# Kernel optimization log

Hardware: AMD Instinct MI355X
Metric: run time of the kernel (lower is better)

Reference implementation:

```python
import jax, jax.numpy as jnp
import numpy as np

C = 256
CK = C // 8  # query/key projection dim

def conv1x1(x, w, b):
    # x: (B,C,H,W), w: (O,C), b: (O,)
    return jnp.einsum('bchw,oc->bohw', x, w) + b[None, :, None, None]

def conv3x3(x, w, b):
    # w: (O,C,3,3)
    y = jax.lax.conv_general_dilated(x, w, window_strides=(1, 1), padding='SAME',
                                     dimension_numbers=('NCHW', 'OIHW', 'NCHW'))
    return y + b[None, :, None, None]

def setup_inputs() -> dict:
    key = jax.random.key(0)
    ks = jax.random.split(key, 24)
    s = 0.05
    d = {
        'x1': jax.random.normal(ks[0], (4, C, 64, 64), jnp.float32),
        'x2': jax.random.normal(ks[1], (4, C, 64, 64), jnp.float32),
        'wq1': jax.random.normal(ks[2], (CK, C), jnp.float32) * s,
        'bq1': jax.random.normal(ks[3], (CK,), jnp.float32) * s,
        'wk1': jax.random.normal(ks[4], (CK, C), jnp.float32) * s,
        'bk1': jax.random.normal(ks[5], (CK,), jnp.float32) * s,
        'wv1': jax.random.normal(ks[6], (C, C), jnp.float32) * s,
        'bv1': jax.random.normal(ks[7], (C,), jnp.float32) * s,
        'wq2': jax.random.normal(ks[8], (CK, C), jnp.float32) * s,
        'bq2': jax.random.normal(ks[9], (CK,), jnp.float32) * s,
        'wk2': jax.random.normal(ks[10], (CK, C), jnp.float32) * s,
        'bk2': jax.random.normal(ks[11], (CK,), jnp.float32) * s,
        'wv2': jax.random.normal(ks[12], (C, C), jnp.float32) * s,
        'bv2': jax.random.normal(ks[13], (C,), jnp.float32) * s,
        'wd1': jax.random.normal(ks[14], (C, C), jnp.float32) * s,
        'bd1': jax.random.normal(ks[15], (C,), jnp.float32) * s,
        'wd3': jax.random.normal(ks[16], (C, C, 3, 3), jnp.float32) * s,
        'bd3': jax.random.normal(ks[17], (C,), jnp.float32) * s,
        'gamma1': jax.random.normal(ks[18], (1,), jnp.float32) * 0.5,
        'gamma2': jax.random.normal(ks[19], (1,), jnp.float32) * 0.5,
    }
    return d

def reference(x1, x2, wq1, bq1, wk1, bk1, wv1, bv1, wq2, bq2, wk2, bk2, wv2, bv2,
              wd1, bd1, wd3, bd3, gamma1, gamma2):
    B, Cc, H, W = x1.shape
    N = H * W
    # projections (1x1 convs), flattened to (B, d, N)
    q1 = conv1x1(x1, wq1, bq1).reshape(B, CK, N)
    k1 = conv1x1(x1, wk1, bk1).reshape(B, CK, N)
    v1 = conv1x1(x1, wv1, bv1).reshape(B, Cc, N)
    q2 = conv1x1(x2, wq2, bq2).reshape(B, CK, N)
    k2 = conv1x1(x2, wk2, bk2).reshape(B, CK, N)
    v2 = conv1x1(x2, wv2, bv2).reshape(B, Cc, N)
    # cross attention 1: queries from x1, keys/values from x2
    energy1 = jnp.einsum('bdi,bdj->bij', q1, k2)          # (B,N,N)
    attn1 = jax.nn.softmax(energy1, axis=-1)
    out1 = jnp.einsum('bcj,bij->bci', v2, attn1).reshape(B, Cc, H, W)
    # cross attention 2: queries from x2, keys/values from x1
    energy2 = jnp.einsum('bdi,bdj->bij', q2, k1)
    attn2 = jax.nn.softmax(energy2, axis=-1)
    out2 = jnp.einsum('bcj,bij->bci', v1, attn2).reshape(B, Cc, H, W)
    # residual conv branches + gamma-scaled skip (norm1/norm2 in source are dead code)
    out1 = out1 + conv1x1(x1, wd1, bd1) + conv3x3(x1, wd3, bd3)
    out2 = out2 + conv1x1(x2, wd1, bd1) + conv3x3(x2, wd3, bd3)
    out1 = x1 + gamma1[0] * out1
    out2 = x2 + gamma2[0] * out2
    return (out1, out2)
```

## Files before the change

### kernel.cpp

```cpp
#include <hip/hip_runtime.h>
#include <hip/hip_bf16.h>

#define CC 256
#define CKD 32
#define NN 4096
#define HH 64
#define WW 64
#define BB 4

#define LOG2E 1.44269504088896f
#define EXPSHIFT 23.0831203874f

typedef __attribute__((ext_vector_type(8))) short short8;
typedef __attribute__((ext_vector_type(4))) float floatx4;

__device__ __forceinline__ unsigned f2bf(float f) {
  union { float f; unsigned u; } v; v.f = f;
  unsigned r = v.u + 0x7fffu + ((v.u >> 16) & 1u);
  return r >> 16;
}
__device__ __forceinline__ unsigned short f2bf_fast(float f) {
  return (unsigned short)((__float_as_uint(f) + 0x8000u) >> 16);
}
__device__ __forceinline__ float fast_exp2(float x) {
#if __has_builtin(__builtin_amdgcn_exp2f)
  return __builtin_amdgcn_exp2f(x);
#else
  return __expf(x * 0.693147181f);
#endif
}

__global__ __launch_bounds__(256) void xpack_kernel(
    const float* __restrict__ x1, const float* __restrict__ x2,
    unsigned short* __restrict__ Xp) {
  const int t = threadIdx.x;
  const int nb = blockIdx.x, cbk = blockIdx.y, img = blockIdx.z;
  const float* X = ((img >> 2) ? x2 : x1) + (size_t)(img & 3) * CC * NN;
  const int n0 = nb * 64, c0 = cbk * 64;
  __shared__ float tile[64][65];
  const int nl = t & 63, cl0 = t >> 6;
#pragma unroll
  for (int i = 0; i < 16; ++i)
    tile[cl0 + i * 4][nl] = X[(size_t)(c0 + cl0 + i * 4) * NN + n0 + nl];
  __syncthreads();
#pragma unroll
  for (int it = 0; it < 2; ++it) {
    int id = it * 256 + t;
    int nl2 = id >> 3, cc = id & 7;
    short8 v;
#pragma unroll
    for (int j = 0; j < 8; ++j) v[j] = (short)f2bf(tile[cc * 8 + j][nl2]);
    *(short8*)(Xp + (size_t)img * NN * CC + (size_t)(n0 + nl2) * CC + c0 + cc * 8) = v;
  }
}

__global__ __launch_bounds__(256) void wpack_kernel(
    const float* __restrict__ wd1, const float* __restrict__ wd3,
    const float* __restrict__ wq1, const float* __restrict__ wk1,
    const float* __restrict__ wv1,
    const float* __restrict__ wq2, const float* __restrict__ wk2,
    const float* __restrict__ wv2,
    const float* __restrict__ bq1, const float* __restrict__ bk1,
    const float* __restrict__ bv1,
    const float* __restrict__ bq2, const float* __restrict__ bk2,
    const float* __restrict__ bv2,
    unsigned short* __restrict__ Wp, unsigned short* __restrict__ Wqkv,
    float* __restrict__ Bias) {
  const int id = blockIdx.x * 256 + threadIdx.x;
#pragma unroll
  for (int tap = 0; tap < 10; ++tap) {
    float v = (tap < 9) ? wd3[(size_t)id * 9 + tap] : wd1[id];
    Wp[(size_t)tap * (CC * CC) + id] = (unsigned short)f2bf(v);
  }
#pragma unroll
  for (int j = 0; j < 3; ++j) {
    int e = id + j * 65536;
    if (e < 2 * 320 * 256) {
      int inp = e / (320 * 256), rem = e % (320 * 256);
      int o = rem >> 8, c = rem & 255;
      float v;
      if (inp == 0)
        v = (o < 32) ? wq1[o * 256 + c] * LOG2E
            : (o < 64) ? wk1[(o - 32) * 256 + c] : wv1[(o - 64) * 256 + c];
      else
        v = (o < 32) ? wq2[o * 256 + c] * LOG2E
            : (o < 64) ? wk2[(o - 32) * 256 + c] : wv2[(o - 64) * 256 + c];
      Wqkv[e] = (unsigned short)f2bf(v);
    }
  }
  if (id < 640) {
    int inp = id / 320, o = id % 320;
    float v;
    if (inp == 0) v = (o < 32) ? bq1[o] * LOG2E
                      : (o < 64) ? bk1[o - 32] : bv1[o - 64];
    else          v = (o < 32) ? bq2[o] * LOG2E
                      : (o < 64) ? bk2[o - 32] : bv2[o - 64];
    Bias[id] = v;
  }
}

__global__ __launch_bounds__(256) void proj_mfma_kernel(
    const unsigned short* __restrict__ Xp, const unsigned short* __restrict__ Wqkv,
    const float* __restrict__ Bias,
    unsigned short* __restrict__ Qp1, unsigned short* __restrict__ Kp1,
    unsigned short* __restrict__ Vp1,
    unsigned short* __restrict__ Qp2, unsigned short* __restrict__ Kp2,
    unsigned short* __restrict__ Vp2) {
  const int t = threadIdx.x;
  const int w = t >> 6, lane = t & 63;
  const int l15 = lane & 15, g = lane >> 4;
  const int img = blockIdx.x, pb = blockIdx.y;
  const int pix0 = pb * 64;
  const int inp = img >> 2, b = img & 3;
  const unsigned short* Xi = Xp + (size_t)img * NN * CC;
  const unsigned short* Wb = Wqkv + (size_t)inp * 320 * CC;
  const float* Bi = Bias + inp * 320;
  unsigned short* Qp = (inp ? Qp2 : Qp1) + (size_t)b * NN * CKD;
  unsigned short* Kp = (inp ? Kp2 : Kp1) + (size_t)b * NN * CKD;
  unsigned short* Vp = (inp ? Vp2 : Vp1) + (size_t)b * NN * CC;

  __shared__ unsigned short tile[320][72];

  floatx4 acc[4][5];
#pragma unroll
  for (int mf = 0; mf < 4; ++mf)
#pragma unroll
    for (int nf = 0; nf < 5; ++nf) acc[mf][nf] = (floatx4){0.f, 0.f, 0.f, 0.f};
  const int o0w = w * 80;

#pragma unroll
  for (int cb = 0; cb < 8; ++cb) {
    short8 a[4], bfr[5];
#pragma unroll
    for (int mf = 0; mf < 4; ++mf)
      a[mf] = *(const short8*)(Xi + (size_t)(pix0 + mf * 16 + l15) * CC + cb * 32 + g * 8);
#pragma unroll
    for (int nf = 0; nf < 5; ++nf)
      bfr[nf] = *(const short8*)(Wb + (size_t)(o0w + nf * 16 + l15) * CC + cb * 32 + g * 8);
#pragma unroll
    for (int nf = 0; nf < 5; ++nf)
#pragma unroll
      for (int mf = 0; mf < 4; ++mf)
        acc[mf][nf] = __builtin_amdgcn_mfma_f32_16x16x32_bf16(
            a[mf], bfr[nf], acc[mf][nf], 0, 0, 0);
  }

#pragma unroll
  for (int nf = 0; nf < 5; ++nf) {
    float bs = Bi[o0w + nf * 16 + l15];
#pragma unroll
    for (int mf = 0; mf < 4; ++mf) {
      uint2 pk;
      pk.x = f2bf(acc[mf][nf][0] + bs) | (f2bf(acc[mf][nf][1] + bs) << 16);
      pk.y = f2bf(acc[mf][nf][2] + bs) | (f2bf(acc[mf][nf][3] + bs) << 16);
      *(uint2*)&tile[o0w + nf * 16 + l15][mf * 16 + g * 4] = pk;
    }
  }
  __syncthreads();

  {
    const int pix = t >> 2, ch = t & 3;
    short8 vq, vk;
#pragma unroll
    for (int e = 0; e < 8; ++e) {
      vq[e] = (short)tile[ch * 8 + e][pix];
      vk[e] = (short)tile[32 + ch * 8 + e][pix];
    }
    *(short8*)(Qp + (size_t)(pix0 + pix) * CKD + ch * 8) = vq;
    *(short8*)(Kp + (size_t)(pix0 + pix) * CKD + ch * 8) = vk;
  }
#pragma unroll
  for (int it = 0; it < 8; ++it) {
    short8 vv = *(const short8*)&tile[64 + t][it * 8];
    *(short8*)(Vp + ((size_t)((pix0 >> 3) + it) * CC + t) * 8) = vv;
  }
}

__global__ __launch_bounds__(256, 2) void conv_mfma_kernel(
    const unsigned short* __restrict__ Xp, const unsigned short* __restrict__ Wp,
    const float* __restrict__ bd1, const float* __restrict__ bd3,
    unsigned short* __restrict__ R1, unsigned short* __restrict__ R2) {
  const int t = threadIdx.x;
  const int w = t >> 6, lane = t & 63;
  const int l15 = lane & 15, g = lane >> 4;
  const int ob = blockIdx.x, img = blockIdx.y, pb = blockIdx.z;
  const int o0 = ob * 128, n0 = pb * 128, y0 = pb * 2;
  const int wm = w >> 1, wn = w & 1;

  const unsigned short* Xi = Xp + (size_t)img * NN * CC;
  unsigned short* R = ((img >> 2) ? R2 : R1) + (size_t)(img & 3) * CC * NN;

  __shared__ unsigned short xs[4][66][72];

  floatx4 acc[4][4];
#pragma unroll
  for (int m = 0; m < 4; ++m)
#pragma unroll
    for (int n = 0; n < 4; ++n) acc[m][n] = (floatx4){0.f, 0.f, 0.f, 0.f};

  for (int cb = 0; cb < 4; ++cb) {
    const int c0 = cb * 64;
    __syncthreads();
#pragma unroll
    for (int it = 0; it < 9; ++it) {
      int id = it * 256 + t;
      if (id < 2112) {
        int r = id / 528, rem = id % 528;
        int col = rem >> 3, cc = rem & 7;
        int y = y0 - 1 + r, x = col - 1;
        short8 v = {0, 0, 0, 0, 0, 0, 0, 0};
        if (y >= 0 && y < HH && x >= 0 && x < WW)
          v = *(const short8*)(Xi + (size_t)(y * WW + x) * CC + c0 + cc * 8);
        *(short8*)&xs[r][col][cc * 8] = v;
      }
    }
    __syncthreads();
#pragma unroll
    for (int tap = 0; tap < 10; ++tap) {
      const int dy = (tap < 9) ? tap / 3 - 1 : 0;
      const int dx = (tap < 9) ? tap % 3 - 1 : 0;
      const int rrow = 1 + wn + dy;
      const unsigned short* wrow =
          Wp + (size_t)(tap * CC + o0 + wm * 64 + l15) * CC + c0 + g * 8;
#pragma unroll
      for (int ks = 0; ks < 2; ++ks) {
        short8 af[4], bf[4];
#pragma unroll
        for (int m = 0; m < 4; ++m)
          af[m] = *(const short8*)(wrow + (size_t)(m * 16) * CC + ks * 32);
#pragma unroll
        for (int n = 0; n < 4; ++n)
          bf[n] = *(const short8*)&xs[rrow][1 + n * 16 + l15 + dx][ks * 32 + g * 8];
#pragma unroll
        for (int m = 0; m < 4; ++m)
#pragma unroll
          for (int n = 0; n < 4; ++n)
            acc[m][n] = __builtin_amdgcn_mfma_f32_16x16x32_bf16(
                af[m], bf[n], acc[m][n], 0, 0, 0);
      }
    }
  }

#pragma unroll
  for (int m = 0; m < 4; ++m) {
    int ob2 = o0 + wm * 64 + m * 16 + g * 4;
    float bs[4];
#pragma unroll
    for (int r = 0; r < 4; ++r) bs[r] = bd1[ob2 + r] + bd3[ob2 + r];
#pragma unroll
    for (int n = 0; n < 4; ++n) {
      int pix = n0 + wn * 64 + n * 16 + l15;
#pragma unroll
      for (int r = 0; r < 4; ++r)
        R[(size_t)(ob2 + r) * NN + pix] = f2bf_fast(acc[m][n][r] + bs[r]);
    }
  }
}

__global__ __launch_bounds__(256, 2) void attn_kernel(
    const unsigned short* __restrict__ Qp1, const unsigned short* __restrict__ Kp1,
    const unsigned short* __restrict__ Qp2, const unsigned short* __restrict__ Kp2,
    const unsigned short* __restrict__ Vp1, const unsigned short* __restrict__ Vp2,
    const unsigned short* __restrict__ R1, const unsigned short* __restrict__ R2,
    const float* __restrict__ x1, const float* __restrict__ x2,
    const float* __restrict__ g1, const float* __restrict__ g2,
    float* __restrict__ out) {
  const int t = threadIdx.x;
  const int w = t >> 6, lane = t & 63;
  const int l15 = lane & 15, g = lane >> 4;
  const int att = blockIdx.x, b = blockIdx.y;
  const int i0 = blockIdx.z * 64;

  const unsigned short *Qp, *Kp, *Vp, *Rb; const float *x; float gamma; float* o;
  if (att == 0) { Qp = Qp1; Kp = Kp2; Vp = Vp2; Rb = R1; x = x1; gamma = g1[0]; o = out; }
  else          { Qp = Qp2; Kp = Kp1; Vp = Vp1; Rb = R2; x = x2; gamma = g2[0];
                  o = out + (size_t)BB * CC * NN; }
  Qp += (size_t)b * NN * CKD; Kp += (size_t)b * NN * CKD; Vp += (size_t)b * NN * CC;
  Rb += (size_t)b * CC * NN; x += (size_t)b * CC * NN; o += (size_t)b * CC * NN;

  __shared__ unsigned short p_s[2][64][72];
  __shared__ float l_s[64];

  short8 bq = *(const short8*)(Qp + (size_t)(i0 + w * 16 + l15) * CKD + g * 8);

  floatx4 acc[4][4];
#pragma unroll
  for (int a = 0; a < 4; ++a)
#pragma unroll
    for (int c = 0; c < 4; ++c) acc[a][c] = (floatx4){0.f, 0.f, 0.f, 0.f};
  float l_acc = 0.f;
  const floatx4 zinit = {-EXPSHIFT, -EXPSHIFT, -EXPSHIFT, -EXPSHIFT};

  short8 kr[2][4], vr[2][8];
#pragma unroll
  for (int js = 0; js < 4; ++js)
    kr[0][js] = *(const short8*)(Kp + (size_t)(js * 16 + l15) * CKD + g * 8);
#pragma unroll
  for (int ks = 0; ks < 2; ++ks)
#pragma unroll
    for (int cs = 0; cs < 4; ++cs)
      vr[0][ks * 4 + cs] = *(const short8*)(Vp +
          ((size_t)(ks * 4 + g) * CC + (w * 64 + cs * 16 + l15)) * 8);

#pragma unroll 2
  for (int jt = 0; jt < NN / 64; ++jt) {
    const int cur = jt & 1, nxt = cur ^ 1;
    if (jt + 1 < NN / 64) {
      const size_t j0n = (size_t)(jt + 1) * 64;
#pragma unroll
      for (int js = 0; js < 4; ++js)
        kr[nxt][js] = *(const short8*)(Kp + (j0n + js * 16 + l15) * CKD + g * 8);
#pragma unroll
      for (int ks = 0; ks < 2; ++ks)
#pragma unroll
        for (int cs = 0; cs < 4; ++cs)
          vr[nxt][ks * 4 + cs] = *(const short8*)(Vp +
              (((j0n >> 3) + ks * 4 + g) * CC + (w * 64 + cs * 16 + l15)) * 8);
    }
#pragma unroll
    for (int js = 0; js < 4; ++js) {
      floatx4 s = __builtin_amdgcn_mfma_f32_16x16x32_bf16(kr[cur][js], bq, zinit, 0, 0, 0);
      float p0 = fast_exp2(s[0]);
      float p1 = fast_exp2(s[1]);
      float p2 = fast_exp2(s[2]);
      float p3 = fast_exp2(s[3]);
      l_acc += (p0 + p1) + (p2 + p3);
      unsigned u0 = __float_as_uint(p0) + 0x8000u;
      unsigned u1 = __float_as_uint(p1) + 0x8000u;
      unsigned u2 = __float_as_uint(p2) + 0x8000u;
      unsigned u3 = __float_as_uint(p3) + 0x8000u;
      uint2 pk;
      pk.x = __builtin_amdgcn_perm(u1, u0, 0x07060302u);
      pk.y = __builtin_amdgcn_perm(u3, u2, 0x07060302u);
      *(uint2*)&p_s[cur][w * 16 + l15][js * 16 + g * 4] = pk;
    }
    __syncthreads();
#pragma unroll
    for (int ks = 0; ks < 2; ++ks) {
      short8 ap[4];
#pragma unroll
      for (int isub = 0; isub < 4; ++isub)
        ap[isub] = *(const short8*)&p_s[cur][isub * 16 + l15][ks * 32 + g * 8];
#pragma unroll
      for (int cs = 0; cs < 4; ++cs)
#pragma unroll
        for (int isub = 0; isub < 4; ++isub)
          acc[isub][cs] = __builtin_amdgcn_mfma_f32_16x16x32_bf16(
              ap[isub], vr[cur][ks * 4 + cs], acc[isub][cs], 0, 0, 0);
    }
  }

  l_acc += __shfl_xor(l_acc, 16);
  l_acc += __shfl_xor(l_acc, 32);
  if (g == 0) l_s[w * 16 + l15] = l_acc;
  __syncthreads();

#pragma unroll
  for (int isub = 0; isub < 4; ++isub) {
    float linv[4];
#pragma unroll
    for (int r = 0; r < 4; ++r) linv[r] = 1.f / l_s[isub * 16 + g * 4 + r];
#pragma unroll
    for (int cs = 0; cs < 4; ++cs) {
      int c = w * 64 + cs * 16 + l15;
      size_t base = (size_t)c * NN + i0 + isub * 16 + g * 4;
      float4 xr = *(const float4*)(x + base);
      uint2 rr = *(const uint2*)(Rb + base);
      float r0 = __uint_as_float(rr.x << 16);
      float r1 = __uint_as_float(rr.x & 0xffff0000u);
      float r2 = __uint_as_float(rr.y << 16);
      float r3 = __uint_as_float(rr.y & 0xffff0000u);
      float4 ov;
      ov.x = xr.x + gamma * (acc[isub][cs][0] * linv[0] + r0);
      ov.y = xr.y + gamma * (acc[isub][cs][1] * linv[1] + r1);
      ov.z = xr.z + gamma * (acc[isub][cs][2] * linv[2] + r2);
      ov.w = xr.w + gamma * (acc[isub][cs][3] * linv[3] + r3);
      *(float4*)(o + base) = ov;
    }
  }
}

extern "C" void kernel_launch(void* const* d_in, const int* in_sizes, int n_in,
                              void* d_out, int out_size, void* d_ws, size_t ws_size,
                              hipStream_t stream) {
  const float* x1  = (const float*)d_in[0];
  const float* x2  = (const float*)d_in[1];
  const float* wq1 = (const float*)d_in[2];
  const float* bq1 = (const float*)d_in[3];
  const float* wk1 = (const float*)d_in[4];
  const float* bk1 = (const float*)d_in[5];
  const float* wv1 = (const float*)d_in[6];
  const float* bv1 = (const float*)d_in[7];
  const float* wq2 = (const float*)d_in[8];
  const float* bq2 = (const float*)d_in[9];
  const float* wk2 = (const float*)d_in[10];
  const float* bk2 = (const float*)d_in[11];
  const float* wv2 = (const float*)d_in[12];
  const float* bv2 = (const float*)d_in[13];
  const float* wd1 = (const float*)d_in[14];
  const float* bd1 = (const float*)d_in[15];
  const float* wd3 = (const float*)d_in[16];
  const float* bd3 = (const float*)d_in[17];
  const float* g1  = (const float*)d_in[18];
  const float* g2  = (const float*)d_in[19];
  float* out = (float*)d_out;

  const size_t QB = (size_t)BB * NN * CKD * 2;
  const size_t VB = (size_t)BB * NN * CC * 2;
  const size_t RB = (size_t)BB * NN * CC * 2;
  const size_t XB = (size_t)2 * BB * NN * CC * 2;
  const size_t WPB = (size_t)10 * CC * CC * 2;
  const size_t WQB = (size_t)2 * 320 * CC * 2;
  char* base = (char*)d_ws;
  unsigned short* R1 = (unsigned short*)(base);
  unsigned short* R2 = (unsigned short*)(base + RB);
  unsigned short* Qp1 = (unsigned short*)(base + 2 * RB);
  unsigned short* Kp1 = (unsigned short*)(base + 2 * RB + QB);
  unsigned short* Qp2 = (unsigned short*)(base + 2 * RB + 2 * QB);
  unsigned short* Kp2 = (unsigned short*)(base + 2 * RB + 3 * QB);
  unsigned short* Vp1 = (unsigned short*)(base + 2 * RB + 4 * QB);
  unsigned short* Vp2 = (unsigned short*)(base + 2 * RB + 4 * QB + VB);
  unsigned short* Xp  = (unsigned short*)(base + 2 * RB + 4 * QB + 2 * VB);
  unsigned short* Wp  = (unsigned short*)(base + 2 * RB + 4 * QB + 2 * VB + XB);
  unsigned short* Wqkv = (unsigned short*)(base + 2 * RB + 4 * QB + 2 * VB + XB + WPB);
  float* Bias = (float*)(base + 2 * RB + 4 * QB + 2 * VB + XB + WPB + WQB);

  xpack_kernel<<<dim3(NN / 64, CC / 64, 2 * BB), 256, 0, stream>>>(x1, x2, Xp);
  wpack_kernel<<<dim3(CC * CC / 256), 256, 0, stream>>>(
      wd1, wd3, wq1, wk1, wv1, wq2, wk2, wv2,
      bq1, bk1, bv1, bq2, bk2, bv2, Wp, Wqkv, Bias);

  proj_mfma_kernel<<<dim3(2 * BB, NN / 64), 256, 0, stream>>>(
      Xp, Wqkv, Bias, Qp1, Kp1, Vp1, Qp2, Kp2, Vp2);

  conv_mfma_kernel<<<dim3(2, 2 * BB, NN / 128), 256, 0, stream>>>(
      Xp, Wp, bd1, bd3, R1, R2);

  attn_kernel<<<dim3(2, BB, NN / 64), 256, 0, stream>>>(
      Qp1, Kp1, Qp2, Kp2, Vp1, Vp2, R1, R2, x1, x2, g1, g2, out);
}
```

Baseline: 316.9 us.

## Fuse 3x3+1x1 conv branch into attention kernel prologue, restructure softmax pipeline

Removes the separate conv kernel and computes the combined conv residual per attention block (one image row of 64 pixels, all 256 output channels) in its prologue. The result is kept in LDS as bf16 and consumed in the epilogue, eliminating the R1/R2 global round trip and one launch. The attention loop is also rewritten into a software-pipelined form where GEMM1 of the next tile overlaps GEMM2 of the current one, with double-buffered K/V registers. The cost is more LDS per block, which may reduce occupancy, and a longer serial prologue in each attention block.

New measurement: 301.5 us. 4.8% less time.

```diff
diff --git a/kernel.cpp b/kernel.cpp
--- a/kernel.cpp
+++ b/kernel.cpp
@@ -19,8 +19,8 @@
   unsigned r = v.u + 0x7fffu + ((v.u >> 16) & 1u);
   return r >> 16;
 }
-__device__ __forceinline__ unsigned short f2bf_fast(float f) {
-  return (unsigned short)((__float_as_uint(f) + 0x8000u) >> 16);
+__device__ __forceinline__ unsigned f2bf_fast(float f) {
+  return (__float_as_uint(f) + 0x8000u) >> 16;
 }
 __device__ __forceinline__ float fast_exp2(float x) {
 #if __has_builtin(__builtin_amdgcn_exp2f)
@@ -29,6 +29,8 @@
   return __expf(x * 0.693147181f);
 #endif
 }
+__device__ __forceinline__ float bf_lo(unsigned u) { return __uint_as_float(u << 16); }
+__device__ __forceinline__ float bf_hi(unsigned u) { return __uint_as_float(u & 0xffff0000u); }
 
 __global__ __launch_bounds__(256) void xpack_kernel(
     const float* __restrict__ x1, const float* __restrict__ x2,
@@ -176,92 +178,12 @@
   }
 }
 
-__global__ __launch_bounds__(256, 2) void conv_mfma_kernel(
-    const unsigned short* __restrict__ Xp, const unsigned short* __restrict__ Wp,
-    const float* __restrict__ bd1, const float* __restrict__ bd3,
-    unsigned short* __restrict__ R1, unsigned short* __restrict__ R2) {
-  const int t = threadIdx.x;
-  const int w = t >> 6, lane = t & 63;
-  const int l15 = lane & 15, g = lane >> 4;
-  const int ob = blockIdx.x, img = blockIdx.y, pb = blockIdx.z;
-  const int o0 = ob * 128, n0 = pb * 128, y0 = pb * 2;
-  const int wm = w >> 1, wn = w & 1;
-
-  const unsigned short* Xi = Xp + (size_t)img * NN * CC;
-  unsigned short* R = ((img >> 2) ? R2 : R1) + (size_t)(img & 3) * CC * NN;
-
-  __shared__ unsigned short xs[4][66][72];
-
-  floatx4 acc[4][4];
-#pragma unroll
-  for (int m = 0; m < 4; ++m)
-#pragma unroll
-    for (int n = 0; n < 4; ++n) acc[m][n] = (floatx4){0.f, 0.f, 0.f, 0.f};
-
-  for (int cb = 0; cb < 4; ++cb) {
-    const int c0 = cb * 64;
-    __syncthreads();
-#pragma unroll
-    for (int it = 0; it < 9; ++it) {
-      int id = it * 256 + t;
-      if (id < 2112) {
-        int r = id / 528, rem = id % 528;
-        int col = rem >> 3, cc = rem & 7;
-        int y = y0 - 1 + r, x = col - 1;
-        short8 v = {0, 0, 0, 0, 0, 0, 0, 0};
-        if (y >= 0 && y < HH && x >= 0 && x < WW)
-          v = *(const short8*)(Xi + (size_t)(y * WW + x) * CC + c0 + cc * 8);
-        *(short8*)&xs[r][col][cc * 8] = v;
-      }
-    }
-    __syncthreads();
-#pragma unroll
-    for (int tap = 0; tap < 10; ++tap) {
-      const int dy = (tap < 9) ? tap / 3 - 1 : 0;
-      const int dx = (tap < 9) ? tap % 3 - 1 : 0;
-      const int rrow = 1 + wn + dy;
-      const unsigned short* wrow =
-          Wp + (size_t)(tap * CC + o0 + wm * 64 + l15) * CC + c0 + g * 8;
-#pragma unroll
-      for (int ks = 0; ks < 2; ++ks) {
-        short8 af[4], bf[4];
-#pragma unroll
-        for (int m = 0; m < 4; ++m)
-          af[m] = *(const short8*)(wrow + (size_t)(m * 16) * CC + ks * 32);
-#pragma unroll
-        for (int n = 0; n < 4; ++n)
-          bf[n] = *(const short8*)&xs[rrow][1 + n * 16 + l15 + dx][ks * 32 + g * 8];
-#pragma unroll
-        for (int m = 0; m < 4; ++m)
-#pragma unroll
-          for (int n = 0; n < 4; ++n)
-            acc[m][n] = __builtin_amdgcn_mfma_f32_16x16x32_bf16(
-                af[m], bf[n], acc[m][n], 0, 0, 0);
-      }
-    }
-  }
-
-#pragma unroll
-  for (int m = 0; m < 4; ++m) {
-    int ob2 = o0 + wm * 64 + m * 16 + g * 4;
-    float bs[4];
-#pragma unroll
-    for (int r = 0; r < 4; ++r) bs[r] = bd1[ob2 + r] + bd3[ob2 + r];
-#pragma unroll
-    for (int n = 0; n < 4; ++n) {
-      int pix = n0 + wn * 64 + n * 16 + l15;
-#pragma unroll
-      for (int r = 0; r < 4; ++r)
-        R[(size_t)(ob2 + r) * NN + pix] = f2bf_fast(acc[m][n][r] + bs[r]);
-    }
-  }
-}
-
 __global__ __launch_bounds__(256, 2) void attn_kernel(
     const unsigned short* __restrict__ Qp1, const unsigned short* __restrict__ Kp1,
     const unsigned short* __restrict__ Qp2, const unsigned short* __restrict__ Kp2,
     const unsigned short* __restrict__ Vp1, const unsigned short* __restrict__ Vp2,
-    const unsigned short* __restrict__ R1, const unsigned short* __restrict__ R2,
+    const unsigned short* __restrict__ Xp, const unsigned short* __restrict__ Wp,
+    const float* __restrict__ bd1, const float* __restrict__ bd3,
     const float* __restrict__ x1, const float* __restrict__ x2,
     const float* __restrict__ g1, const float* __restrict__ g2,
     float* __restrict__ out) {
@@ -269,16 +191,22 @@
   const int w = t >> 6, lane = t & 63;
   const int l15 = lane & 15, g = lane >> 4;
   const int att = blockIdx.x, b = blockIdx.y;
-  const int i0 = blockIdx.z * 64;
-
-  const unsigned short *Qp, *Kp, *Vp, *Rb; const float *x; float gamma; float* o;
-  if (att == 0) { Qp = Qp1; Kp = Kp2; Vp = Vp2; Rb = R1; x = x1; gamma = g1[0]; o = out; }
-  else          { Qp = Qp2; Kp = Kp1; Vp = Vp1; Rb = R2; x = x2; gamma = g2[0];
+  const int yblk = blockIdx.z;
+  const int i0 = yblk * 64;
+
+  const unsigned short *Qp, *Kp, *Vp; const float *x; float gamma; float* o;
+  if (att == 0) { Qp = Qp1; Kp = Kp2; Vp = Vp2; x = x1; gamma = g1[0]; o = out; }
+  else          { Qp = Qp2; Kp = Kp1; Vp = Vp1; x = x2; gamma = g2[0];
                   o = out + (size_t)BB * CC * NN; }
   Qp += (size_t)b * NN * CKD; Kp += (size_t)b * NN * CKD; Vp += (size_t)b * NN * CC;
-  Rb += (size_t)b * CC * NN; x += (size_t)b * CC * NN; o += (size_t)b * CC * NN;
-
-  __shared__ unsigned short p_s[2][64][72];
+  x += (size_t)b * CC * NN; o += (size_t)b * CC * NN;
+  const unsigned short* Xi = Xp + (size_t)(att * 4 + b) * NN * CC;
+
+  __shared__ union {
+    unsigned short xs[3][66][72];
+    unsigned short ps[2][64][72];
+  } u;
+  __shared__ unsigned short cres[256][68];
   __shared__ float l_s[64];
 
   short8 bq = *(const short8*)(Qp + (size_t)(i0 + w * 16 + l15) * CKD + g * 8);
@@ -292,34 +220,23 @@
   const floatx4 zinit = {-EXPSHIFT, -EXPSHIFT, -EXPSHIFT, -EXPSHIFT};
 
   short8 kr[2][4], vr[2][8];
-#pragma unroll
-  for (int js = 0; js < 4; ++js)
-    kr[0][js] = *(const short8*)(Kp + (size_t)(js * 16 + l15) * CKD + g * 8);
-#pragma unroll
-  for (int ks = 0; ks < 2; ++ks)
-#pragma unroll
-    for (int cs = 0; cs < 4; ++cs)
-      vr[0][ks * 4 + cs] = *(const short8*)(Vp +
-          ((size_t)(ks * 4 + g) * CC + (w * 64 + cs * 16 + l15)) * 8);
-
-#pragma unroll 2
-  for (int jt = 0; jt < NN / 64; ++jt) {
-    const int cur = jt & 1, nxt = cur ^ 1;
-    if (jt + 1 < NN / 64) {
-      const size_t j0n = (size_t)(jt + 1) * 64;
-#pragma unroll
-      for (int js = 0; js < 4; ++js)
-        kr[nxt][js] = *(const short8*)(Kp + (j0n + js * 16 + l15) * CKD + g * 8);
-#pragma unroll
-      for (int ks = 0; ks < 2; ++ks)
-#pragma unroll
-        for (int cs = 0; cs < 4; ++cs)
-          vr[nxt][ks * 4 + cs] = *(const short8*)(Vp +
-              (((j0n >> 3) + ks * 4 + g) * CC + (w * 64 + cs * 16 + l15)) * 8);
-    }
+  auto LOADK = [&](int tt, short8* d) {
+    const unsigned short* kb = Kp + ((size_t)tt * 64 + l15) * CKD + g * 8;
+#pragma unroll
+    for (int js = 0; js < 4; ++js) d[js] = *(const short8*)(kb + js * 16 * CKD);
+  };
+  auto LOADV = [&](int tt, short8* d) {
+#pragma unroll
+    for (int ks = 0; ks < 2; ++ks)
+#pragma unroll
+      for (int cs = 0; cs < 4; ++cs)
+        d[ks * 4 + cs] = *(const short8*)(Vp +
+            (((size_t)tt * 8 + ks * 4 + g) * CC + (w * 64 + cs * 16 + l15)) * 8);
+  };
+  auto GEMM1 = [&](const short8* kb, unsigned short (*ps)[72]) {
 #pragma unroll
     for (int js = 0; js < 4; ++js) {
-      floatx4 s = __builtin_amdgcn_mfma_f32_16x16x32_bf16(kr[cur][js], bq, zinit, 0, 0, 0);
+      floatx4 s = __builtin_amdgcn_mfma_f32_16x16x32_bf16(kb[js], bq, zinit, 0, 0, 0);
       float p0 = fast_exp2(s[0]);
       float p1 = fast_exp2(s[1]);
       float p2 = fast_exp2(s[2]);
@@ -332,22 +249,103 @@
       uint2 pk;
       pk.x = __builtin_amdgcn_perm(u1, u0, 0x07060302u);
       pk.y = __builtin_amdgcn_perm(u3, u2, 0x07060302u);
-      *(uint2*)&p_s[cur][w * 16 + l15][js * 16 + g * 4] = pk;
-    }
-    __syncthreads();
+      *(uint2*)&ps[w * 16 + l15][js * 16 + g * 4] = pk;
+    }
+  };
+  auto GEMM2 = [&](const short8* vb, unsigned short (*ps)[72]) {
 #pragma unroll
     for (int ks = 0; ks < 2; ++ks) {
       short8 ap[4];
 #pragma unroll
       for (int isub = 0; isub < 4; ++isub)
-        ap[isub] = *(const short8*)&p_s[cur][isub * 16 + l15][ks * 32 + g * 8];
+        ap[isub] = *(const short8*)&ps[isub * 16 + l15][ks * 32 + g * 8];
 #pragma unroll
       for (int cs = 0; cs < 4; ++cs)
 #pragma unroll
         for (int isub = 0; isub < 4; ++isub)
           acc[isub][cs] = __builtin_amdgcn_mfma_f32_16x16x32_bf16(
-              ap[isub], vr[cur][ks * 4 + cs], acc[isub][cs], 0, 0, 0);
-    }
+              ap[isub], vb[ks * 4 + cs], acc[isub][cs], 0, 0, 0);
+    }
+  };
+
+  LOADK(0, kr[0]); LOADK(1, kr[1]); LOADV(0, vr[0]);
+
+  {
+    floatx4 ac[4][4];
+#pragma unroll
+    for (int pm = 0; pm < 4; ++pm)
+#pragma unroll
+      for (int on = 0; on < 4; ++on) ac[pm][on] = (floatx4){0.f, 0.f, 0.f, 0.f};
+
+    for (int cb = 0; cb < 4; ++cb) {
+      const int c0 = cb * 64;
+      if (cb) __syncthreads();
+#pragma unroll
+      for (int it = 0; it < 7; ++it) {
+        int id = it * 256 + t;
+        if (id < 1584) {
+          int r = id / 528, rem = id % 528;
+          int col = rem >> 3, cc = rem & 7;
+          int y = yblk - 1 + r, xx = col - 1;
+          short8 v = {0, 0, 0, 0, 0, 0, 0, 0};
+          if (y >= 0 && y < HH && xx >= 0 && xx < WW)
+            v = *(const short8*)(Xi + (size_t)(y * WW + xx) * CC + c0 + cc * 8);
+          *(short8*)&u.xs[r][col][cc * 8] = v;
+        }
+      }
+      __syncthreads();
+#pragma unroll
+      for (int tap = 0; tap < 10; ++tap) {
+        const int dy = (tap < 9) ? tap / 3 - 1 : 0;
+        const int dx = (tap < 9) ? tap % 3 - 1 : 0;
+        const unsigned short* wrow =
+            Wp + ((size_t)tap * CC + w * 64 + l15) * CC + c0 + g * 8;
+#pragma unroll
+        for (int ks = 0; ks < 2; ++ks) {
+          short8 af[4], bw[4];
+#pragma unroll
+          for (int pm = 0; pm < 4; ++pm)
+            af[pm] = *(const short8*)&u.xs[1 + dy][1 + pm * 16 + l15 + dx][ks * 32 + g * 8];
+#pragma unroll
+          for (int on = 0; on < 4; ++on)
+            bw[on] = *(const short8*)(wrow + (size_t)(on * 16) * CC + ks * 32);
+#pragma unroll
+          for (int pm = 0; pm < 4; ++pm)
+#pragma unroll
+            for (int on = 0; on < 4; ++on)
+              ac[pm][on] = __builtin_amdgcn_mfma_f32_16x16x32_bf16(
+                  af[pm], bw[on], ac[pm][on], 0, 0, 0);
+        }
+      }
+    }
+#pragma unroll
+    for (int on = 0; on < 4; ++on) {
+      int oo = w * 64 + on * 16 + l15;
+      float bs = bd1[oo] + bd3[oo];
+#pragma unroll
+      for (int pm = 0; pm < 4; ++pm) {
+        uint2 pk;
+        pk.x = f2bf_fast(ac[pm][on][0] + bs) | (f2bf_fast(ac[pm][on][1] + bs) << 16);
+        pk.y = f2bf_fast(ac[pm][on][2] + bs) | (f2bf_fast(ac[pm][on][3] + bs) << 16);
+        *(uint2*)&cres[oo][pm * 16 + g * 4] = pk;
+      }
+    }
+  }
+  __syncthreads();
+
+  GEMM1(kr[0], u.ps[0]);
+  __syncthreads();
+
+  for (int jt = 0; jt < 64; jt += 2) {
+    if (jt + 2 < 64) LOADK(jt + 2, kr[0]);
+    LOADV(jt + 1, vr[1]);
+    GEMM1(kr[1], u.ps[1]);
+    GEMM2(vr[0], u.ps[0]);
+    __syncthreads();
+    if (jt + 3 < 64) LOADK(jt + 3, kr[1]);
+    if (jt + 2 < 64) { LOADV(jt + 2, vr[0]); GEMM1(kr[0], u.ps[0]); }
+    GEMM2(vr[1], u.ps[1]);
+    __syncthreads();
   }
 
   l_acc += __shfl_xor(l_acc, 16);
@@ -365,16 +363,12 @@
       int c = w * 64 + cs * 16 + l15;
       size_t base = (size_t)c * NN + i0 + isub * 16 + g * 4;
       float4 xr = *(const float4*)(x + base);
-      uint2 rr = *(const uint2*)(Rb + base);
-      float r0 = __uint_as_float(rr.x << 16);
-      float r1 = __uint_as_float(rr.x & 0xffff0000u);
-      float r2 = __uint_as_float(rr.y << 16);
-      float r3 = __uint_as_float(rr.y & 0xffff0000u);
+      uint2 cr = *(const uint2*)&cres[c][isub * 16 + g * 4];
       float4 ov;
-      ov.x = xr.x + gamma * (acc[isub][cs][0] * linv[0] + r0);
-      ov.y = xr.y + gamma * (acc[isub][cs][1] * linv[1] + r1);
-      ov.z = xr.z + gamma * (acc[isub][cs][2] * linv[2] + r2);
-      ov.w = xr.w + gamma * (acc[isub][cs][3] * linv[3] + r3);
+      ov.x = xr.x + gamma * (acc[isub][cs][0] * linv[0] + bf_lo(cr.x));
+      ov.y = xr.y + gamma * (acc[isub][cs][1] * linv[1] + bf_hi(cr.x));
+      ov.z = xr.z + gamma * (acc[isub][cs][2] * linv[2] + bf_lo(cr.y));
+      ov.w = xr.w + gamma * (acc[isub][cs][3] * linv[3] + bf_hi(cr.y));
       *(float4*)(o + base) = ov;
     }
   }
@@ -407,23 +401,20 @@
 
   const size_t QB = (size_t)BB * NN * CKD * 2;
   const size_t VB = (size_t)BB * NN * CC * 2;
-  const size_t RB = (size_t)BB * NN * CC * 2;
   const size_t XB = (size_t)2 * BB * NN * CC * 2;
   const size_t WPB = (size_t)10 * CC * CC * 2;
   const size_t WQB = (size_t)2 * 320 * CC * 2;
   char* base = (char*)d_ws;
-  unsigned short* R1 = (unsigned short*)(base);
-  unsigned short* R2 = (unsigned short*)(base + RB);
-  unsigned short* Qp1 = (unsigned short*)(base + 2 * RB);
-  unsigned short* Kp1 = (unsigned short*)(base + 2 * RB + QB);
-  unsigned short* Qp2 = (unsigned short*)(base + 2 * RB + 2 * QB);
-  unsigned short* Kp2 = (unsigned short*)(base + 2 * RB + 3 * QB);
-  unsigned short* Vp1 = (unsigned short*)(base + 2 * RB + 4 * QB);
-  unsigned short* Vp2 = (unsigned short*)(base + 2 * RB + 4 * QB + VB);
-  unsigned short* Xp  = (unsigned short*)(base + 2 * RB + 4 * QB + 2 * VB);
-  unsigned short* Wp  = (unsigned short*)(base + 2 * RB + 4 * QB + 2 * VB + XB);
-  unsigned short* Wqkv = (unsigned short*)(base + 2 * RB + 4 * QB + 2 * VB + XB + WPB);
-  float* Bias = (float*)(base + 2 * RB + 4 * QB + 2 * VB + XB + WPB + WQB);
+  unsigned short* Qp1 = (unsigned short*)(base);
+  unsigned short* Kp1 = (unsigned short*)(base + QB);
+  unsigned short* Qp2 = (unsigned short*)(base + 2 * QB);
+  unsigned short* Kp2 = (unsigned short*)(base + 3 * QB);
+  unsigned short* Vp1 = (unsigned short*)(base + 4 * QB);
+  unsigned short* Vp2 = (unsigned short*)(base + 4 * QB + VB);
+  unsigned short* Xp  = (unsigned short*)(base + 4 * QB + 2 * VB);
+  unsigned short* Wp  = (unsigned short*)(base + 4 * QB + 2 * VB + XB);
+  unsigned short* Wqkv = (unsigned short*)(base + 4 * QB + 2 * VB + XB + WPB);
+  float* Bias = (float*)(base + 4 * QB + 2 * VB + XB + WPB + WQB);
 
   xpack_kernel<<<dim3(NN / 64, CC / 64, 2 * BB), 256, 0, stream>>>(x1, x2, Xp);
   wpack_kernel<<<dim3(CC * CC / 256), 256, 0, stream>>>(
@@ -433,9 +424,6 @@
   proj_mfma_kernel<<<dim3(2 * BB, NN / 64), 256, 0, stream>>>(
       Xp, Wqkv, Bias, Qp1, Kp1, Vp1, Qp2, Kp2, Vp2);
 
-  conv_mfma_kernel<<<dim3(2, 2 * BB, NN / 128), 256, 0, stream>>>(
-      Xp, Wp, bd1, bd3, R1, R2);
-
   attn_kernel<<<dim3(2, BB, NN / 64), 256, 0, stream>>>(
-      Qp1, Kp1, Qp2, Kp2, Vp1, Vp2, R1, R2, x1, x2, g1, g2, out);
-}
+      Qp1, Kp1, Qp2, Kp2, Vp1, Vp2, Xp, Wp, bd1, bd3, x1, x2, g1, g2, out);
+}
```
